# Optimization experiments

Measured on AMD Instinct MI355X. Metric: run time of the kernel, lower is better.

Reference implementation:

```python
import jax, jax.numpy as jnp
import numpy as np


def _conv(x, w, pad):
    # NCHW conv, stride 1
    return jax.lax.conv_general_dilated(
        x, w, window_strides=(1, 1), padding=pad,
        dimension_numbers=('NCHW', 'OIHW', 'NCHW'))


def setup_inputs() -> dict:
    key = jax.random.key(0)
    ks = jax.random.split(key, 8)
    N, Cin, H, W = 8, 512, 64, 64
    Cout, scale = 128, 2
    sd = 0.02
    return {
        'x':     jax.random.normal(ks[0], (N, Cin, H, W), jnp.float32),
        'w_du':  jax.random.normal(ks[1], (Cout, Cin, 3, 1), jnp.float32) * sd,
        'b_du':  jnp.zeros((Cout,), jnp.float32),
        'w_lr':  jax.random.normal(ks[2], (Cout, Cin, 1, 3), jnp.float32) * sd,
        'b_lr':  jnp.zeros((Cout,), jnp.float32),
        'w_1x1': jax.random.normal(ks[3], (Cout, Cin, 1, 1), jnp.float32) * sd,
        'w_ch':  jax.random.normal(ks[4], (Cout, 3 * Cout, 1, 1), jnp.float32) * sd,
        'w_w':   jax.random.normal(ks[5], (Cout * scale, Cout, 1, 1), jnp.float32) * sd,
        'w_H':   jax.random.normal(ks[6], (Cout * scale, Cout, 1, 1), jnp.float32) * sd,
        'scale': scale,
    }


def _conv_du(x, w, b):
    # convDU3, stride=1: the (3,1) conv is applied to each 1-tall row slice with
    # padding (1,0); rows are folded into the batch dim (vectorized, same math).
    N, C, H, W = x.shape
    rows = x.transpose(0, 2, 1, 3).reshape(N * H, C, 1, W)
    y = _conv(rows, w, ((1, 1), (0, 0))) + b[None, :, None, None]
    y = jax.nn.relu(y)                       # (N*H, Cout, 1, W)
    Co = y.shape[1]
    return y.reshape(N, H, Co, W).transpose(0, 2, 1, 3)


def _conv_lr(x, w, b):
    # convLR3, stride=1: (1,3) conv per 1-wide column slice; columns -> batch.
    N, C, H, W = x.shape
    cols = x.transpose(0, 3, 1, 2).reshape(N * W, C, H, 1)
    y = _conv(cols, w, ((0, 0), (1, 1))) + b[None, :, None, None]
    y = jax.nn.relu(y)                       # (N*W, Cout, H, 1)
    Co = y.shape[1]
    return y.reshape(N, W, Co, H).transpose(0, 2, 3, 1)


def reference(x, w_du, b_du, w_lr, b_lr, w_1x1, w_ch, w_w, w_H, scale):
    xdu = _conv_du(x, w_du, b_du)
    xlr = _conv_lr(x, w_lr, b_lr)
    x1 = _conv(x, w_1x1, ((0, 0), (0, 0)))
    x = jnp.concatenate((x1, xlr, xdu), axis=1)
    x = _conv(x, w_ch, ((0, 0), (0, 0)))
    x = _conv(x, w_w, ((0, 0), (0, 0)))      # (N, Cout*scale, H, W)
    N, C, H, W = x.shape
    # height pixel-shuffle: channels -> height
    xp = x.transpose(0, 3, 2, 1).reshape(N, W, H * scale, C // scale)
    xp = xp.transpose(0, 3, 2, 1)            # (N, Cout, H*scale, W)
    xh = _conv(xp, w_H, ((0, 0), (0, 0)))    # (N, Cout*scale, H*scale, W)
    # width pixel-shuffle: channels -> width
    xh = xh.transpose(0, 2, 3, 1).reshape(N, H * scale, W * scale, C // scale)
    return xh.transpose(0, 3, 1, 2)          # (N, Cout, H*scale, W*scale)
```

## Files before the change

kernel.cpp:

```cpp
#include <hip/hip_runtime.h>
#include <hip/hip_bf16.h>
#include <stdint.h>
#include <stddef.h>


typedef __attribute__((ext_vector_type(8))) __bf16 bf16x8;
typedef __attribute__((ext_vector_type(4))) float  f32x4;
typedef __attribute__((ext_vector_type(2))) float  f32x2;
typedef __attribute__((ext_vector_type(4))) unsigned int u32x4;
typedef __attribute__((ext_vector_type(2))) unsigned int u32x2;

#define BAR() asm volatile("s_waitcnt lgkmcnt(0)\n\ts_barrier" ::: "memory")



__global__ __launch_bounds__(256) void prep_k(
    const float* __restrict__ w_ch, const float* __restrict__ w_1x1,
    const float* __restrict__ w_lr, const float* __restrict__ w_du,
    const float* __restrict__ w_H,  const float* __restrict__ w_w,
    __bf16* __restrict__ Wf, __bf16* __restrict__ W2f)
{
  __shared__ float wh[2][128];
  __shared__ float Mrow[2][128];
  int bid = blockIdx.x;
  if (bid < 768) {
    int gid = bid * 256 + threadIdx.x;
    int r = gid >> 9, c = gid & 511;
    float v;
    if (r < 128) {
      const float* a_ = w_ch + r * 384;
      const float* b_ = w_1x1 + c;
      float s0 = 0.f, s1 = 0.f, s2 = 0.f, s3 = 0.f;
      #pragma unroll
      for (int j = 0; j < 128; j += 4) {
        s0 += a_[j + 0] * b_[(size_t)(j + 0) * 512];
        s1 += a_[j + 1] * b_[(size_t)(j + 1) * 512];
        s2 += a_[j + 2] * b_[(size_t)(j + 2) * 512];
        s3 += a_[j + 3] * b_[(size_t)(j + 3) * 512];
      }
      v = (s0 + s1) + (s2 + s3);
    } else if (r < 256) {
      v = w_lr[(r - 128) * 1536 + c * 3 + 1];
    } else {
      v = w_du[(r - 256) * 1536 + c * 3 + 1];
    }
    int gks = c >> 5, lsub = (c >> 3) & 3, jj = c & 7;
    int mfrag = r >> 4, lrow = r & 15;
    Wf[((gks * 24 + mfrag) << 9) + ((lrow + 16 * lsub) << 3) + jj] = (__bf16)v;
  } else {
    int t = threadIdx.x & 127, half = threadIdx.x >> 7;
    int r = (bid - 768) * 2 + half;
    int beta = r >> 8, gam = r & 1, irow = (r >> 1) & 127;
    wh[half][t] = w_H[(gam * 128 + irow) * 128 + t];
    __syncthreads();
    {
      const float* ww = w_w + beta * 16384 + t;
      float s0 = 0.f, s1 = 0.f, s2 = 0.f, s3 = 0.f;
      #pragma unroll
      for (int s = 0; s < 128; s += 4) {
        s0 += wh[half][s + 0] * ww[(s + 0) * 128];
        s1 += wh[half][s + 1] * ww[(s + 1) * 128];
        s2 += wh[half][s + 2] * ww[(s + 2) * 128];
        s3 += wh[half][s + 3] * ww[(s + 3) * 128];
      }
      Mrow[half][t] = (s0 + s1) + (s2 + s3);
    }
    __syncthreads();
    int mfrag = r >> 4, lrow = r & 15;
    #pragma unroll
    for (int c0 = 0; c0 < 384; c0 += 128) {
      int col = c0 + t;
      float v;
      if (c0 == 0) {
        v = Mrow[half][t];
      } else {
        const float* wc = w_ch + col;
        float s0 = 0.f, s1 = 0.f, s2 = 0.f, s3 = 0.f;
        #pragma unroll
        for (int k = 0; k < 128; k += 4) {
          s0 += Mrow[half][k + 0] * wc[(k + 0) * 384];
          s1 += Mrow[half][k + 1] * wc[(k + 1) * 384];
          s2 += Mrow[half][k + 2] * wc[(k + 2) * 384];
          s3 += Mrow[half][k + 3] * wc[(k + 3) * 384];
        }
        v = (s0 + s1) + (s2 + s3);
      }
      int gks = col >> 5, lsub = (col >> 3) & 3, jj = col & 7;
      W2f[((gks * 32 + mfrag) << 9) + ((lrow + 16 * lsub) << 3) + jj] = (__bf16)v;
    }
  }
}


__device__ __forceinline__ int swzB(int px) {
  return (((px & 7) ^ ((px >> 3) & 7)) << 4);
}

__global__ __launch_bounds__(512, 4) void fused_k(
    const float* __restrict__ x, const __bf16* __restrict__ Wf,
    const __bf16* __restrict__ W2f,
    const float* __restrict__ b_lr, const float* __restrict__ b_du,
    float* __restrict__ out)
{
  __shared__ __align__(16) char smem[49152 + 16384];
  char* Tlds = smem;
  char* buf0 = smem + 49152;
  char* buf1 = smem + 49152 + 8192;

  const int tid  = threadIdx.x;
  const int lane = tid & 63;
  const int wv   = tid >> 6;
  const int l15  = lane & 15, lg = lane >> 4;

  const int p0      = blockIdx.x * 64;
  const int img     = p0 >> 12;
  const int pixbase = p0 & 4095;
  const float* xb   = x + (size_t)img * (512 * 4096) + pixbase;
  const char* Wfb   = (const char*)Wf;
  const char* W2b   = (const char*)W2f;

  const int sp4 = (tid & 15) * 4;
  const int skp = (tid >> 4) * 2;

  auto issueS = [&](int kt, f32x4* ldv) {
    ldv[0] = *(const f32x4*)(xb + (size_t)(kt * 64 + skp) * 4096 + sp4);
    ldv[1] = *(const f32x4*)(xb + (size_t)(kt * 64 + skp + 1) * 4096 + sp4);
  };
  auto writeS = [&](const f32x4* ldv, char* bw) {
    #pragma unroll
    for (int pi = 0; pi < 4; ++pi) {
      int px = sp4 + pi;
      union { __bf16 b[2]; unsigned int u; } wd;
      wd.b[0] = (__bf16)ldv[0][pi];
      wd.b[1] = (__bf16)ldv[1][pi];
      *(unsigned int*)(bw + px * 128 + ((skp * 2) ^ swzB(px))) = wd.u;
    }
  };

  f32x4 acc1[3][4] = {};

  auto compute1 = [&](int kt, const char* bbuf) {
    bf16x8 af[2][3];
    #pragma unroll
    for (int ks = 0; ks < 2; ++ks)
      #pragma unroll
      for (int i = 0; i < 3; ++i)
        af[ks][i] = *(const bf16x8*)(Wfb +
            (((kt * 2 + ks) * 24 + wv * 3 + i) << 10) + lane * 16);
    #pragma unroll
    for (int ks = 0; ks < 2; ++ks) {
      bf16x8 bfr[4];
      #pragma unroll
      for (int j = 0; j < 4; ++j) {
        int rb = j * 16 + l15;
        bfr[j] = *(const bf16x8*)(bbuf + rb * 128 +
                                  ((ks * 64 + lg * 16) ^ swzB(rb)));
      }
      #pragma unroll
      for (int i = 0; i < 3; ++i)
        #pragma unroll
        for (int j = 0; j < 4; ++j)
          acc1[i][j] = __builtin_amdgcn_mfma_f32_16x16x32_bf16(
              af[ks][i], bfr[j], acc1[i][j], 0, 0, 0);
    }
  };

  f32x4 ldA[2], ldB[2];
  issueS(0, ldA);
  issueS(1, ldB);
  writeS(ldA, buf0);
  BAR();

  #pragma unroll 1
  for (int kt2 = 0; kt2 < 8; kt2 += 2) {
    if (kt2 < 6) issueS(kt2 + 2, ldA);
    compute1(kt2, buf0);
    writeS(ldB, buf1);
    BAR();
    if (kt2 < 5) issueS(kt2 + 3, ldB);
    compute1(kt2 + 1, buf1);
    if (kt2 < 6) { writeS(ldA, buf0); BAR(); }
  }

  #pragma unroll
  for (int i = 0; i < 3; ++i) {
    int m0 = wv * 48 + i * 16 + lg * 4;
    bool rl = (m0 >= 128);
    const float* bp = (m0 >= 256) ? (b_du + (m0 - 256)) : (b_lr + (m0 - 128));
    float b0 = 0.f, b1 = 0.f, b2 = 0.f, b3 = 0.f;
    if (rl) { b0 = bp[0]; b1 = bp[1]; b2 = bp[2]; b3 = bp[3]; }
    #pragma unroll
    for (int j = 0; j < 4; ++j) {
      int p = j * 16 + l15;
      union { __bf16 b[4]; u32x2 u; } wd;
      float v0 = acc1[i][j][0], v1 = acc1[i][j][1];
      float v2 = acc1[i][j][2], v3 = acc1[i][j][3];
      if (rl) {
        v0 = fmaxf(v0 + b0, 0.f); v1 = fmaxf(v1 + b1, 0.f);
        v2 = fmaxf(v2 + b2, 0.f); v3 = fmaxf(v3 + b3, 0.f);
      }
      wd.b[0] = (__bf16)v0; wd.b[1] = (__bf16)v1;
      wd.b[2] = (__bf16)v2; wd.b[3] = (__bf16)v3;
      *(u32x2*)(Tlds + p * 768 + ((m0 * 2) ^ ((p & 7) << 4))) = wd.u;
    }
  }
  BAR();

  f32x4 acc2[4][4] = {};
  bf16x8 afA[4], afB[4];
  #pragma unroll
  for (int i = 0; i < 4; ++i)
    afA[i] = *(const bf16x8*)(W2b + ((0 * 32 + wv * 4 + i) << 10) + lane * 16);

  #pragma unroll 1
  for (int g2 = 0; g2 < 6; ++g2) {
    int gA = 2 * g2, gB = 2 * g2 + 1;
    #pragma unroll
    for (int i = 0; i < 4; ++i)
      afB[i] = *(const bf16x8*)(W2b + ((gB * 32 + wv * 4 + i) << 10) + lane * 16);
    {
      bf16x8 bfr[4];
      #pragma unroll
      for (int j = 0; j < 4; ++j) {
        int rb = j * 16 + l15;
        bfr[j] = *(const bf16x8*)(Tlds + rb * 768 +
                                  ((gA * 64 + lg * 16) ^ ((rb & 7) << 4)));
      }
      #pragma unroll
      for (int i = 0; i < 4; ++i)
        #pragma unroll
        for (int j = 0; j < 4; ++j)
          acc2[i][j] = __builtin_amdgcn_mfma_f32_16x16x32_bf16(
              afA[i], bfr[j], acc2[i][j], 0, 0, 0);
    }
    if (g2 < 5) {
      #pragma unroll
      for (int i = 0; i < 4; ++i)
        afA[i] = *(const bf16x8*)(W2b + (((gA + 2) * 32 + wv * 4 + i) << 10) + lane * 16);
    }
    {
      bf16x8 bfr[4];
      #pragma unroll
      for (int j = 0; j < 4; ++j) {
        int rb = j * 16 + l15;
        bfr[j] = *(const bf16x8*)(Tlds + rb * 768 +
                                  ((gB * 64 + lg * 16) ^ ((rb & 7) << 4)));
      }
      #pragma unroll
      for (int i = 0; i < 4; ++i)
        #pragma unroll
        for (int j = 0; j < 4; ++j)
          acc2[i][j] = __builtin_amdgcn_mfma_f32_16x16x32_bf16(
              afB[i], bfr[j], acc2[i][j], 0, 0, 0);
    }
  }

  #pragma unroll
  for (int i = 0; i < 4; ++i) {
    int r = (wv * 4 + i) * 16 + lg * 4;
    int beta = r >> 8;
    int irow = (r >> 1) & 127;
    #pragma unroll
    for (int j = 0; j < 4; ++j) {
      int pp = pixbase + j * 16 + l15;
      int h = pp >> 6, w = pp & 63;
      size_t o0 = ((((size_t)img * 128 + irow) * 128) + (2 * h + beta)) * 128
                  + 2 * w;
      f32x2 lo; lo.x = acc2[i][j][0]; lo.y = acc2[i][j][1];
      f32x2 hi; hi.x = acc2[i][j][2]; hi.y = acc2[i][j][3];
      *(f32x2*)(out + o0)         = lo;
      *(f32x2*)(out + o0 + 16384) = hi;
    }
  }
}


extern "C" void kernel_launch(void* const* d_in, const int* in_sizes, int n_in,
                              void* d_out, int out_size, void* d_ws, size_t ws_size,
                              hipStream_t stream) {
  const float* x     = (const float*)d_in[0];
  const float* w_du  = (const float*)d_in[1];
  const float* b_du  = (const float*)d_in[2];
  const float* w_lr  = (const float*)d_in[3];
  const float* b_lr  = (const float*)d_in[4];
  const float* w_1x1 = (const float*)d_in[5];
  const float* w_ch  = (const float*)d_in[6];
  const float* w_w   = (const float*)d_in[7];
  const float* w_H   = (const float*)d_in[8];
  float* out = (float*)d_out;

  char* ws = (char*)d_ws;
  __bf16* Wf  = (__bf16*)(ws + 0);
  __bf16* W2f = (__bf16*)(ws + 393216);
  if (ws_size < (size_t)786432) return;

  prep_k <<<1024, 256, 0, stream>>>(w_ch, w_1x1, w_lr, w_du, w_H, w_w, Wf, W2f);
  fused_k<<<512, 512, 0, stream>>>(x, Wf, W2f, b_lr, b_du, out);
}
```

Measured before the change: 51.95 us.

## Double pixel tile to 128 per block and rework stage-1 staging pipeline

```diff
diff --git a/kernel.cpp b/kernel.cpp
--- a/kernel.cpp
+++ b/kernel.cpp
@@ -92,94 +92,96 @@
 }
 
 
-__device__ __forceinline__ int swzB(int px) {
-  return (((px & 7) ^ ((px >> 3) & 7)) << 4);
+__device__ __forceinline__ int slotS(int px) {
+  return ((px & 3) ^ ((px >> 2) & 3) ^ ((px >> 4) & 3)) << 4;
 }
 
-__global__ __launch_bounds__(512, 4) void fused_k(
+__global__ __launch_bounds__(512, 2) void fused_k(
     const float* __restrict__ x, const __bf16* __restrict__ Wf,
     const __bf16* __restrict__ W2f,
     const float* __restrict__ b_lr, const float* __restrict__ b_du,
     float* __restrict__ out)
 {
-  __shared__ __align__(16) char smem[49152 + 16384];
+  __shared__ __align__(16) char smem[98304 + 16384];
   char* Tlds = smem;
-  char* buf0 = smem + 49152;
-  char* buf1 = smem + 49152 + 8192;
+  char* buf0 = smem + 98304;
+  char* buf1 = smem + 98304 + 8192;
 
   const int tid  = threadIdx.x;
   const int lane = tid & 63;
   const int wv   = tid >> 6;
   const int l15  = lane & 15, lg = lane >> 4;
 
-  const int p0      = blockIdx.x * 64;
+  const int p0      = blockIdx.x * 128;
   const int img     = p0 >> 12;
   const int pixbase = p0 & 4095;
   const float* xb   = x + (size_t)img * (512 * 4096) + pixbase;
   const char* Wfb   = (const char*)Wf;
   const char* W2b   = (const char*)W2f;
 
-  const int sp4 = (tid & 15) * 4;
-  const int skp = (tid >> 4) * 2;
-
-  auto issueS = [&](int kt, f32x4* ldv) {
-    ldv[0] = *(const f32x4*)(xb + (size_t)(kt * 64 + skp) * 4096 + sp4);
-    ldv[1] = *(const f32x4*)(xb + (size_t)(kt * 64 + skp + 1) * 4096 + sp4);
+  const int s_px = tid & 127;
+  const int s_k8 = (tid >> 7) * 8;
+
+  float ldA[8], ldB[8];
+  auto issueS = [&](int kt, float* ldv) {
+    #pragma unroll
+    for (int j = 0; j < 8; ++j)
+      ldv[j] = xb[(size_t)(kt * 32 + s_k8 + j) * 4096 + s_px];
   };
-  auto writeS = [&](const f32x4* ldv, char* bw) {
-    #pragma unroll
-    for (int pi = 0; pi < 4; ++pi) {
-      int px = sp4 + pi;
-      union { __bf16 b[2]; unsigned int u; } wd;
-      wd.b[0] = (__bf16)ldv[0][pi];
-      wd.b[1] = (__bf16)ldv[1][pi];
-      *(unsigned int*)(bw + px * 128 + ((skp * 2) ^ swzB(px))) = wd.u;
-    }
+  auto writeS = [&](const float* ldv, char* bw) {
+    union { __bf16 b[8]; u32x4 u; } wd;
+    #pragma unroll
+    for (int j = 0; j < 8; ++j) wd.b[j] = (__bf16)ldv[j];
+    *(u32x4*)(bw + s_px * 64 + ((s_k8 * 2) ^ slotS(s_px))) = wd.u;
   };
 
-  f32x4 acc1[3][4] = {};
-
-  auto compute1 = [&](int kt, const char* bbuf) {
-    bf16x8 af[2][3];
-    #pragma unroll
-    for (int ks = 0; ks < 2; ++ks)
-      #pragma unroll
-      for (int i = 0; i < 3; ++i)
-        af[ks][i] = *(const bf16x8*)(Wfb +
-            (((kt * 2 + ks) * 24 + wv * 3 + i) << 10) + lane * 16);
-    #pragma unroll
-    for (int ks = 0; ks < 2; ++ks) {
-      bf16x8 bfr[4];
-      #pragma unroll
-      for (int j = 0; j < 4; ++j) {
-        int rb = j * 16 + l15;
-        bfr[j] = *(const bf16x8*)(bbuf + rb * 128 +
-                                  ((ks * 64 + lg * 16) ^ swzB(rb)));
-      }
-      #pragma unroll
-      for (int i = 0; i < 3; ++i)
-        #pragma unroll
-        for (int j = 0; j < 4; ++j)
-          acc1[i][j] = __builtin_amdgcn_mfma_f32_16x16x32_bf16(
-              af[ks][i], bfr[j], acc1[i][j], 0, 0, 0);
-    }
+  f32x4 acc1[3][8] = {};
+  bf16x8 afA[3], afB[3];
+
+  auto loadAf1 = [&](int kt, bf16x8* af) {
+    #pragma unroll
+    for (int i = 0; i < 3; ++i)
+      af[i] = *(const bf16x8*)(Wfb + ((kt * 24 + wv * 3 + i) << 10) + lane * 16);
   };
-
-  f32x4 ldA[2], ldB[2];
+  auto compute1 = [&](const bf16x8* af, const char* bbuf) {
+    bf16x8 bfr[8];
+    #pragma unroll
+    for (int j = 0; j < 8; ++j) {
+      int rb = j * 16 + l15;
+      bfr[j] = *(const bf16x8*)(bbuf + rb * 64 + ((lg * 16) ^ slotS(rb)));
+    }
+    __builtin_amdgcn_s_setprio(1);
+    #pragma unroll
+    for (int i = 0; i < 3; ++i)
+      #pragma unroll
+      for (int j = 0; j < 8; ++j)
+        acc1[i][j] = __builtin_amdgcn_mfma_f32_16x16x32_bf16(
+            af[i], bfr[j], acc1[i][j], 0, 0, 0);
+    __builtin_amdgcn_s_setprio(0);
+  };
+
   issueS(0, ldA);
   issueS(1, ldB);
   writeS(ldA, buf0);
+  issueS(2, ldA);
+  loadAf1(0, afA);
+  loadAf1(1, afB);
   BAR();
 
   #pragma unroll 1
-  for (int kt2 = 0; kt2 < 8; kt2 += 2) {
-    if (kt2 < 6) issueS(kt2 + 2, ldA);
-    compute1(kt2, buf0);
+  for (int kt2 = 0; kt2 < 16; kt2 += 2) {
+    compute1(afA, buf0);
+    if (kt2 < 14) loadAf1(kt2 + 2, afA);
     writeS(ldB, buf1);
+    if (kt2 < 14) issueS(kt2 + 3, ldB);
     BAR();
-    if (kt2 < 5) issueS(kt2 + 3, ldB);
-    compute1(kt2 + 1, buf1);
-    if (kt2 < 6) { writeS(ldA, buf0); BAR(); }
+    compute1(afB, buf1);
+    if (kt2 < 14) {
+      loadAf1(kt2 + 3, afB);
+      writeS(ldA, buf0);
+      if (kt2 < 12) issueS(kt2 + 4, ldA);
+      BAR();
+    }
   }
 
   #pragma unroll
@@ -190,7 +192,7 @@
     float b0 = 0.f, b1 = 0.f, b2 = 0.f, b3 = 0.f;
     if (rl) { b0 = bp[0]; b1 = bp[1]; b2 = bp[2]; b3 = bp[3]; }
     #pragma unroll
-    for (int j = 0; j < 4; ++j) {
+    for (int j = 0; j < 8; ++j) {
       int p = j * 16 + l15;
       union { __bf16 b[4]; u32x2 u; } wd;
       float v0 = acc1[i][j][0], v1 = acc1[i][j][1];
@@ -204,64 +206,72 @@
       *(u32x2*)(Tlds + p * 768 + ((m0 * 2) ^ ((p & 7) << 4))) = wd.u;
     }
   }
-  BAR();
-
-  f32x4 acc2[4][4] = {};
-  bf16x8 afA[4], afB[4];
+  f32x4 acc2[4][8] = {};
+  bf16x8 af2A[4], af2B[4];
   #pragma unroll
   for (int i = 0; i < 4; ++i)
-    afA[i] = *(const bf16x8*)(W2b + ((0 * 32 + wv * 4 + i) << 10) + lane * 16);
+    af2A[i] = *(const bf16x8*)(W2b + ((0 * 32 + wv * 4 + i) << 10) + lane * 16);
+  #pragma unroll
+  for (int i = 0; i < 4; ++i)
+    af2B[i] = *(const bf16x8*)(W2b + ((1 * 32 + wv * 4 + i) << 10) + lane * 16);
+  BAR();
 
   #pragma unroll 1
   for (int g2 = 0; g2 < 6; ++g2) {
     int gA = 2 * g2, gB = 2 * g2 + 1;
-    #pragma unroll
-    for (int i = 0; i < 4; ++i)
-      afB[i] = *(const bf16x8*)(W2b + ((gB * 32 + wv * 4 + i) << 10) + lane * 16);
     {
-      bf16x8 bfr[4];
-      #pragma unroll
-      for (int j = 0; j < 4; ++j) {
+      bf16x8 bfr[8];
+      #pragma unroll
+      for (int j = 0; j < 8; ++j) {
         int rb = j * 16 + l15;
         bfr[j] = *(const bf16x8*)(Tlds + rb * 768 +
                                   ((gA * 64 + lg * 16) ^ ((rb & 7) << 4)));
       }
+      __builtin_amdgcn_s_setprio(1);
       #pragma unroll
       for (int i = 0; i < 4; ++i)
         #pragma unroll
-        for (int j = 0; j < 4; ++j)
+        for (int j = 0; j < 8; ++j)
           acc2[i][j] = __builtin_amdgcn_mfma_f32_16x16x32_bf16(
-              afA[i], bfr[j], acc2[i][j], 0, 0, 0);
+              af2A[i], bfr[j], acc2[i][j], 0, 0, 0);
+      __builtin_amdgcn_s_setprio(0);
     }
     if (g2 < 5) {
       #pragma unroll
       for (int i = 0; i < 4; ++i)
-        afA[i] = *(const bf16x8*)(W2b + (((gA + 2) * 32 + wv * 4 + i) << 10) + lane * 16);
+        af2A[i] = *(const bf16x8*)(W2b + (((gA + 2) * 32 + wv * 4 + i) << 10) + lane * 16);
     }
     {
-      bf16x8 bfr[4];
-      #pragma unroll
-      for (int j = 0; j < 4; ++j) {
+      bf16x8 bfr[8];
+      #pragma unroll
+      for (int j = 0; j < 8; ++j) {
         int rb = j * 16 + l15;
         bfr[j] = *(const bf16x8*)(Tlds + rb * 768 +
                                   ((gB * 64 + lg * 16) ^ ((rb & 7) << 4)));
       }
+      __builtin_amdgcn_s_setprio(1);
       #pragma unroll
       for (int i = 0; i < 4; ++i)
         #pragma unroll
-        for (int j = 0; j < 4; ++j)
+        for (int j = 0; j < 8; ++j)
           acc2[i][j] = __builtin_amdgcn_mfma_f32_16x16x32_bf16(
-              afB[i], bfr[j], acc2[i][j], 0, 0, 0);
+              af2B[i], bfr[j], acc2[i][j], 0, 0, 0);
+      __builtin_amdgcn_s_setprio(0);
+    }
+    if (g2 < 5) {
+      #pragma unroll
+      for (int i = 0; i < 4; ++i)
+        af2B[i] = *(const bf16x8*)(W2b + (((gB + 2) * 32 + wv * 4 + i) << 10) + lane * 16);
     }
   }
 
   #pragma unroll
   for (int i = 0; i < 4; ++i) {
-    int r = (wv * 4 + i) * 16 + lg * 4;
+    int r = wv * 64 + i * 16 + lg * 4;
     int beta = r >> 8;
     int irow = (r >> 1) & 127;
     #pragma unroll
-    for (int j = 0; j < 4; ++j) {
+    for (int j = 0; j < 8; ++j) {
       int pp = pixbase + j * 16 + l15;
       int h = pp >> 6, w = pp & 63;
       size_t o0 = ((((size_t)img * 128 + irow) * 128) + (2 * h + beta)) * 128
@@ -295,5 +305,5 @@
   if (ws_size < (size_t)786432) return;
 
   prep_k <<<1024, 256, 0, stream>>>(w_ch, w_1x1, w_lr, w_du, w_H, w_w, Wf, W2f);
-  fused_k<<<512, 512, 0, stream>>>(x, Wf, W2f, b_lr, b_du, out);
+  fused_k<<<256, 512, 0, stream>>>(x, Wf, W2f, b_lr, b_du, out);
 }
```

Result: faster. 47.82 us (-7.9%).
